# Optimization experiments

Measured on AMD Instinct MI355X. Metric: run time of the kernel, lower is better.

The kernel has to match this reference:

```python
import jax, jax.numpy as jnp
import numpy as np

N_NODES, N_EDGES, D_IN, D_HID, D_OUT = 100000, 3200000, 128, 64, 10


def _gcn_norm(src, dst, n):
    # symmetric normalization deg^{-1/2}[src] * deg^{-1/2}[dst]; edge weights = 1
    ones = jnp.ones(src.shape[0], jnp.float32)
    deg = jax.ops.segment_sum(ones, dst, num_segments=n)
    dinv = jnp.where(deg > 0, jax.lax.rsqrt(jnp.maximum(deg, 1.0)), 0.0)
    return dinv[src] * dinv[dst]


def _gcn_conv(x, W, b, src, dst, norm, n):
    h = x @ W                                   # [N, out]
    msg = norm[:, None] * jnp.take(h, src, axis=0)  # [E+N, out]
    return jax.ops.segment_sum(msg, dst, num_segments=n) + b


def setup_inputs() -> dict:
    key = jax.random.key(0)
    ks = jax.random.split(key, 8)
    x = jax.random.normal(ks[0], (N_NODES, D_IN), jnp.float32)
    edge_index = jax.random.randint(ks[1], (2, N_EDGES), 0, N_NODES, jnp.int32)
    def glorot(k, fan_in, fan_out):
        s = (6.0 / (fan_in + fan_out)) ** 0.5
        return jax.random.uniform(k, (fan_in, fan_out), jnp.float32, -s, s)
    return {
        "x": x,
        "edge_index": edge_index,
        "W1": glorot(ks[2], D_IN, D_HID), "b1": jnp.zeros((D_HID,), jnp.float32),
        "W2": glorot(ks[3], D_HID, D_HID), "b2": jnp.zeros((D_HID,), jnp.float32),
        "W3": glorot(ks[4], D_HID, D_OUT), "b3": jnp.zeros((D_OUT,), jnp.float32),
    }


def reference(x, edge_index, W1, b1, W2, b2, W3, b3):
    n = x.shape[0]
    loops = jnp.arange(n, dtype=edge_index.dtype)
    src = jnp.concatenate([edge_index[0], loops])  # add self-loops (PyG default)
    dst = jnp.concatenate([edge_index[1], loops])
    norm = _gcn_norm(src, dst, n)                  # identical for all 3 layers
    h = jax.nn.relu(_gcn_conv(x, W1, b1, src, dst, norm, n))
    h = jax.nn.relu(_gcn_conv(h, W2, b2, src, dst, norm, n))
    return _gcn_conv(h, W3, b3, src, dst, norm, n)
```

## Files before the change

kernel.cpp:

```cpp
#include <hip/hip_runtime.h>


constexpr int BK_SHIFT = 6;
constexpr int BK_NODES = 64;
constexpr int BK_CAP   = 2432;
constexpr int MAXNB    = 1568;

typedef __attribute__((ext_vector_type(8))) short short8_t;
typedef __attribute__((ext_vector_type(4))) float f32x4_t;

__device__ __forceinline__ unsigned short f2bf(float f) {
    unsigned u = __builtin_bit_cast(unsigned, f);
    u += 0x7FFF + ((u >> 16) & 1);
    return (unsigned short)(u >> 16);
}
__device__ __forceinline__ unsigned pack2(float lo, float hi) {
    return (unsigned)f2bf(lo) | ((unsigned)f2bf(hi) << 16);
}
__device__ __forceinline__ float bf_lo(unsigned d) {
    return __builtin_bit_cast(float, d << 16);
}
__device__ __forceinline__ float bf_hi(unsigned d) {
    return __builtin_bit_cast(float, d & 0xFFFF0000u);
}

__global__ void k_cursor_init(int* __restrict__ cursor, int nb) {
    int i = blockIdx.x * blockDim.x + threadIdx.x;
    if (i < nb) cursor[i] = i * BK_CAP;
}

__global__ void k_partition(const int* __restrict__ src, const int* __restrict__ dst,
                            int E, int nb, int* __restrict__ cursor,
                            unsigned* __restrict__ inter) {
    __shared__ int lcount[MAXNB];
    __shared__ int gbase[MAXNB];
    int t = threadIdx.x;
    int base = blockIdx.x * 16384;
    for (int i = t; i < MAXNB; i += 512) lcount[i] = 0;
    __syncthreads();
    int sv[32], dvv[32];
#pragma unroll
    for (int j = 0; j < 32; j++) {
        int idx = base + j * 512 + t;
        if (idx < E) {
            sv[j] = src[idx]; dvv[j] = dst[idx];
            atomicAdd(&lcount[dvv[j] >> BK_SHIFT], 1);
        } else dvv[j] = -1;
    }
    __syncthreads();
    for (int i = t; i < nb; i += 512) {
        int c = lcount[i]; int g = 0;
        if (c) g = atomicAdd(&cursor[i], c);
        gbase[i] = g; lcount[i] = 0;
    }
    __syncthreads();
#pragma unroll
    for (int j = 0; j < 32; j++) {
        if (dvv[j] >= 0) {
            int b = dvv[j] >> BK_SHIFT;
            int r = atomicAdd(&lcount[b], 1);
            int pos = gbase[b] + r;
            if (pos < (b + 1) * BK_CAP)
                inter[pos] = (unsigned)sv[j] | ((unsigned)(dvv[j] & (BK_NODES - 1)) << 20);
        }
    }
}

__global__ void k_dinvb(const unsigned* __restrict__ inter, const int* __restrict__ cursor,
                        float* __restrict__ dinv, int N) {
    __shared__ int hist[BK_NODES];
    int t = threadIdx.x, b = blockIdx.x;
    if (t < BK_NODES) hist[t] = 0;
    __syncthreads();
    int start = b * BK_CAP;
    int cnt = min(cursor[b] - start, BK_CAP);
    for (int i = t; i < cnt; i += 256) atomicAdd(&hist[inter[start + i] >> 20], 1);
    __syncthreads();
    if (t < BK_NODES) {
        int d = b * BK_NODES + t;
        if (d < N) dinv[d] = rsqrtf((float)(hist[t] + 1));
    }
}

template <int K, bool IN_F32>
__global__ __launch_bounds__(256) void k_gemmMF(const void* __restrict__ Xv,
                           const float* __restrict__ W,
                           const float* __restrict__ dinv,
                           unsigned short* __restrict__ Y, int n) {
    constexpr int KP = K + 8;
    __shared__ unsigned short Al[64 * KP];
    __shared__ unsigned short Bl[64 * KP];
    int t = threadIdx.x;
    int nb = blockIdx.x * 64;
    if (IN_F32) {
        const float* X = (const float*)Xv;
        for (int i = t * 4; i < 64 * K; i += 1024) {
            int r = i / K, c = i % K;
            int node = nb + r;
            float4 v = {0.f, 0.f, 0.f, 0.f};
            if (node < n) v = *reinterpret_cast<const float4*>(X + (size_t)node * K + c);
            uint2 pk = {pack2(v.x, v.y), pack2(v.z, v.w)};
            *reinterpret_cast<uint2*>(&Al[r * KP + c]) = pk;
        }
    } else {
        const unsigned short* X = (const unsigned short*)Xv;
        for (int i = t * 4; i < 64 * K; i += 1024) {
            int r = i / K, c = i % K;
            int node = nb + r;
            uint2 pk = {0u, 0u};
            if (node < n) pk = *reinterpret_cast<const uint2*>(X + (size_t)node * K + c);
            *reinterpret_cast<uint2*>(&Al[r * KP + c]) = pk;
        }
    }
    {
        int c = t & 63, kb = t >> 6;
        for (int k = kb; k < K; k += 4)
            Bl[c * KP + k] = f2bf(W[k * 64 + c]);
    }
    __syncthreads();
    int w = t >> 6, lane = t & 63;
    int ml = lane & 15, kg = lane >> 4;
    f32x4_t acc[4] = {{0,0,0,0},{0,0,0,0},{0,0,0,0},{0,0,0,0}};
    for (int ks = 0; ks < K / 32; ks++) {
        int ko = ks * 32 + kg * 8;
        short8_t a = *reinterpret_cast<const short8_t*>(&Al[(16 * w + ml) * KP + ko]);
#pragma unroll
        for (int c = 0; c < 4; c++) {
            short8_t b = *reinterpret_cast<const short8_t*>(&Bl[(16 * c + ml) * KP + ko]);
            acc[c] = __builtin_amdgcn_mfma_f32_16x16x32_bf16(a, b, acc[c], 0, 0, 0);
        }
    }
#pragma unroll
    for (int r = 0; r < 4; r++) {
        int grow = nb + 16 * w + kg * 4 + r;
        if (grow < n) {
            float dv = dinv[grow];
#pragma unroll
            for (int c = 0; c < 4; c++)
                Y[(size_t)grow * 64 + 16 * c + ml] = f2bf(dv * acc[c][r]);
        }
    }
}

__global__ void k_gemm10(const float* __restrict__ X, const float* __restrict__ W,
                         const float* __restrict__ dinv, float* __restrict__ Y, int n) {
    __shared__ float ws[64 * 10];
    __shared__ float xs[16 * 64];
    int t = threadIdx.x;
    for (int i = t; i < 640; i += 256) ws[i] = W[i];
    int nb = blockIdx.x * 16;
    for (int i = t; i < 16 * 64; i += 256) {
        int r = i >> 6, c = i & 63;
        int node = nb + r;
        xs[i] = (node < n) ? X[(size_t)node * 64 + c] : 0.f;
    }
    __syncthreads();
    int ns = t >> 4, c = t & 15;
    if (c < 10) {
        float acc = 0.f;
        for (int k = 0; k < 64; k++) acc += xs[ns * 64 + k] * ws[k * 10 + c];
        int node = nb + ns;
        if (node < n) Y[(size_t)node * 10 + c] = dinv[node] * acc;
    }
}

template <int OBF>
__global__ __launch_bounds__(512) void k_agg64(const unsigned short* __restrict__ H,
                        const unsigned* __restrict__ inter, const int* __restrict__ cursor,
                        const float* __restrict__ bias, void* __restrict__ outv,
                        int N, int relu) {
    __shared__ unsigned raw[BK_CAP];
    __shared__ unsigned srt[BK_CAP];
    __shared__ int hist[BK_NODES];
    __shared__ int offs[BK_NODES + 1];
    __shared__ int cur[BK_NODES];
    int t = threadIdx.x, b = blockIdx.x;
    if (t < BK_NODES) hist[t] = 0;
    __syncthreads();
    int start = b * BK_CAP;
    int cnt = min(cursor[b] - start, BK_CAP);
    for (int i = t; i < cnt; i += 512) {
        unsigned r = inter[start + i];
        raw[i] = r;
        atomicAdd(&hist[r >> 20], 1);
    }
    __syncthreads();
    if (t < BK_NODES) {
        int v = hist[t];
        int inc = v;
#pragma unroll
        for (int d = 1; d < 64; d <<= 1) {
            int o = __shfl_up(inc, d);
            if (t >= d) inc += o;
        }
        offs[t + 1] = inc;
        if (t == 0) offs[0] = 0;
        cur[t] = inc - v;
    }
    __syncthreads();
    for (int i = t; i < cnt; i += 512) {
        unsigned r = raw[i];
        int pos = atomicAdd(&cur[r >> 20], 1);
        srt[pos] = r & 0xFFFFFu;
    }
    __syncthreads();
    int wv = t >> 6, lane = t & 63;
    int esub = lane >> 3, cg = lane & 7;
    const unsigned short* Hc = H + (cg << 3);
    for (int nd = wv; nd < BK_NODES; nd += 8) {
        int d = b * BK_NODES + nd;
        if (d >= N) break;
        int o0 = offs[nd], o1 = offs[nd + 1];
        float a0 = 0.f, a1 = 0.f, a2 = 0.f, a3 = 0.f;
        float a4 = 0.f, a5 = 0.f, a6 = 0.f, a7 = 0.f;
        int e = o0 + esub;
        for (; e + 24 < o1; e += 32) {
            int s0 = srt[e], s1 = srt[e + 8], s2 = srt[e + 16], s3 = srt[e + 24];
            const uint4 v0 = *reinterpret_cast<const uint4*>(Hc + ((size_t)s0 << 6));
            const uint4 v1 = *reinterpret_cast<const uint4*>(Hc + ((size_t)s1 << 6));
            const uint4 v2 = *reinterpret_cast<const uint4*>(Hc + ((size_t)s2 << 6));
            const uint4 v3 = *reinterpret_cast<const uint4*>(Hc + ((size_t)s3 << 6));
            a0 += bf_lo(v0.x); a1 += bf_hi(v0.x); a2 += bf_lo(v0.y); a3 += bf_hi(v0.y);
            a4 += bf_lo(v0.z); a5 += bf_hi(v0.z); a6 += bf_lo(v0.w); a7 += bf_hi(v0.w);
            a0 += bf_lo(v1.x); a1 += bf_hi(v1.x); a2 += bf_lo(v1.y); a3 += bf_hi(v1.y);
            a4 += bf_lo(v1.z); a5 += bf_hi(v1.z); a6 += bf_lo(v1.w); a7 += bf_hi(v1.w);
            a0 += bf_lo(v2.x); a1 += bf_hi(v2.x); a2 += bf_lo(v2.y); a3 += bf_hi(v2.y);
            a4 += bf_lo(v2.z); a5 += bf_hi(v2.z); a6 += bf_lo(v2.w); a7 += bf_hi(v2.w);
            a0 += bf_lo(v3.x); a1 += bf_hi(v3.x); a2 += bf_lo(v3.y); a3 += bf_hi(v3.y);
            a4 += bf_lo(v3.z); a5 += bf_hi(v3.z); a6 += bf_lo(v3.w); a7 += bf_hi(v3.w);
        }
        for (; e < o1; e += 8) {
            int s0 = srt[e];
            const uint4 v0 = *reinterpret_cast<const uint4*>(Hc + ((size_t)s0 << 6));
            a0 += bf_lo(v0.x); a1 += bf_hi(v0.x); a2 += bf_lo(v0.y); a3 += bf_hi(v0.y);
            a4 += bf_lo(v0.z); a5 += bf_hi(v0.z); a6 += bf_lo(v0.w); a7 += bf_hi(v0.w);
        }
#pragma unroll
        for (int m = 8; m <= 32; m <<= 1) {
            a0 += __shfl_xor(a0, m); a1 += __shfl_xor(a1, m);
            a2 += __shfl_xor(a2, m); a3 += __shfl_xor(a3, m);
            a4 += __shfl_xor(a4, m); a5 += __shfl_xor(a5, m);
            a6 += __shfl_xor(a6, m); a7 += __shfl_xor(a7, m);
        }
        if (esub == 0) {
            float dv = rsqrtf((float)(hist[nd] + 1));
            const uint4 sv = *reinterpret_cast<const uint4*>(Hc + ((size_t)d << 6));
            float s[8] = {bf_lo(sv.x), bf_hi(sv.x), bf_lo(sv.y), bf_hi(sv.y),
                          bf_lo(sv.z), bf_hi(sv.z), bf_lo(sv.w), bf_hi(sv.w)};
            float acc[8] = {a0, a1, a2, a3, a4, a5, a6, a7};
            const float* bp = bias + cg * 8;
            float o[8];
#pragma unroll
            for (int j = 0; j < 8; j++) {
                float val = dv * (acc[j] + s[j]) + bp[j];
                if (relu) val = fmaxf(val, 0.f);
                o[j] = val;
            }
            if (OBF) {
                unsigned short* op = (unsigned short*)outv + (size_t)d * 64 + cg * 8;
                uint4 pk = {pack2(o[0], o[1]), pack2(o[2], o[3]),
                            pack2(o[4], o[5]), pack2(o[6], o[7])};
                *reinterpret_cast<uint4*>(op) = pk;
            } else {
                float* op = (float*)outv + (size_t)d * 64 + cg * 8;
                float4 r0 = {o[0], o[1], o[2], o[3]}, r1 = {o[4], o[5], o[6], o[7]};
                *reinterpret_cast<float4*>(op)     = r0;
                *reinterpret_cast<float4*>(op + 4) = r1;
            }
        }
    }
}

__global__ __launch_bounds__(512) void k_agg10(const float* __restrict__ H,
                        const unsigned* __restrict__ inter, const int* __restrict__ cursor,
                        const float* __restrict__ b3, float* __restrict__ out, int N) {
    __shared__ unsigned raw[BK_CAP];
    __shared__ unsigned srt[BK_CAP];
    __shared__ int hist[BK_NODES];
    __shared__ int offs[BK_NODES + 1];
    __shared__ int cur[BK_NODES];
    int t = threadIdx.x, b = blockIdx.x;
    if (t < BK_NODES) hist[t] = 0;
    __syncthreads();
    int start = b * BK_CAP;
    int cnt = min(cursor[b] - start, BK_CAP);
    for (int i = t; i < cnt; i += 512) {
        unsigned r = inter[start + i];
        raw[i] = r;
        atomicAdd(&hist[r >> 20], 1);
    }
    __syncthreads();
    if (t < BK_NODES) {
        int v = hist[t];
        int inc = v;
#pragma unroll
        for (int d = 1; d < 64; d <<= 1) {
            int o = __shfl_up(inc, d);
            if (t >= d) inc += o;
        }
        offs[t + 1] = inc;
        if (t == 0) offs[0] = 0;
        cur[t] = inc - v;
    }
    __syncthreads();
    for (int i = t; i < cnt; i += 512) {
        unsigned r = raw[i];
        int pos = atomicAdd(&cur[r >> 20], 1);
        srt[pos] = r & 0xFFFFFu;
    }
    __syncthreads();
    int wv = t >> 6, lane = t & 63;
    int esub = lane >> 4, c = lane & 15;
    for (int nd = wv; nd < BK_NODES; nd += 8) {
        int d = b * BK_NODES + nd;
        if (d >= N) break;
        int o0 = offs[nd], o1 = offs[nd + 1];
        float acc = 0.f;
        if (c < 10) {
            int e = o0 + esub;
            for (; e + 12 < o1; e += 16) {
                int s0 = srt[e], s1 = srt[e + 4], s2 = srt[e + 8], s3 = srt[e + 12];
                float h0 = H[(size_t)s0 * 10 + c], h1 = H[(size_t)s1 * 10 + c];
                float h2 = H[(size_t)s2 * 10 + c], h3 = H[(size_t)s3 * 10 + c];
                acc += (h0 + h1) + (h2 + h3);
            }
            for (; e < o1; e += 4) acc += H[(size_t)srt[e] * 10 + c];
        }
        acc += __shfl_xor(acc, 16);
        acc += __shfl_xor(acc, 32);
        if (esub == 0 && c < 10) {
            float dv = rsqrtf((float)(hist[nd] + 1));
            out[(size_t)d * 10 + c] = dv * (acc + H[(size_t)d * 10 + c]) + b3[c];
        }
    }
}

extern "C" void kernel_launch(void* const* d_in, const int* in_sizes, int n_in,
                              void* d_out, int out_size, void* d_ws, size_t ws_size,
                              hipStream_t stream) {
    const float* x  = (const float*)d_in[0];
    const int*   ei = (const int*)d_in[1];
    const float* W1 = (const float*)d_in[2];
    const float* b1 = (const float*)d_in[3];
    const float* W2 = (const float*)d_in[4];
    const float* b2 = (const float*)d_in[5];
    const float* W3 = (const float*)d_in[6];
    const float* b3 = (const float*)d_in[7];

    int N = in_sizes[0] / 128;
    int E = in_sizes[1] / 2;
    const int* esrc = ei;
    const int* edst = ei + E;
    int nb = (N + BK_NODES - 1) >> BK_SHIFT;

    char* p = (char*)d_ws;
    auto carve = [&](size_t bytes) -> void* {
        void* r = p;
        p += (bytes + 255) & ~(size_t)255;
        return r;
    };
    int*      cursor = (int*)carve((size_t)MAXNB * 4);
    unsigned* inter  = (unsigned*)carve((size_t)nb * BK_CAP * 4);
    float*    dinv   = (float*)carve((size_t)N * 4);
    unsigned short* Hs = (unsigned short*)carve((size_t)N * 64 * 2);
    unsigned short* Gb = (unsigned short*)carve((size_t)N * 64 * 2);
    float*    Gf     = (float*)carve((size_t)N * 64 * 4);
    float*    Hs10   = (float*)carve((size_t)N * 10 * 4);
    (void)ws_size; (void)n_in; (void)out_size;

    k_cursor_init<<<(nb + 255) / 256, 256, 0, stream>>>(cursor, nb);
    k_partition<<<(E + 16383) / 16384, 512, 0, stream>>>(esrc, edst, E, nb, cursor, inter);
    k_dinvb<<<nb, 256, 0, stream>>>(inter, cursor, dinv, N);

    k_gemmMF<128, true><<<(N + 63) / 64, 256, 0, stream>>>(x, W1, dinv, Hs, N);
    k_agg64<1><<<nb, 512, 0, stream>>>(Hs, inter, cursor, b1, Gb, N, 1);
    k_gemmMF<64, false><<<(N + 63) / 64, 256, 0, stream>>>(Gb, W2, dinv, Hs, N);
    k_agg64<0><<<nb, 512, 0, stream>>>(Hs, inter, cursor, b2, Gf, N, 1);
    k_gemm10<<<(N + 15) / 16, 256, 0, stream>>>(Gf, W3, dinv, Hs10, N);
    k_agg10<<<nb, 512, 0, stream>>>(Hs10, inter, cursor, b3, (float*)d_out, N);
}
```

Before: 254.1 us.

## Store layer-3 features in bf16, memset cursors, reduce agg unrolling

Stores the 10-wide layer-3 transformed features as bf16 instead of fp32, halving the bytes gathered per edge in the final aggregation. The cursor-init kernel is replaced by a memset, with bucket offsets now computed relative to each bucket base. The gather loops in the 64-wide and 10-wide aggregation kernels are unrolled less, which lowers register pressure but leaves fewer loads in flight. The bf16 features add rounding error to the final layer.

Result: faster. 246.0 us (-3.2%).

```diff
diff --git a/kernel.cpp b/kernel.cpp
--- a/kernel.cpp
+++ b/kernel.cpp
@@ -23,10 +23,8 @@
 __device__ __forceinline__ float bf_hi(unsigned d) {
     return __builtin_bit_cast(float, d & 0xFFFF0000u);
 }
-
-__global__ void k_cursor_init(int* __restrict__ cursor, int nb) {
-    int i = blockIdx.x * blockDim.x + threadIdx.x;
-    if (i < nb) cursor[i] = i * BK_CAP;
+__device__ __forceinline__ float bf1(unsigned short u) {
+    return __builtin_bit_cast(float, (unsigned)u << 16);
 }
 
 __global__ void k_partition(const int* __restrict__ src, const int* __restrict__ dst,
@@ -58,10 +56,10 @@
     for (int j = 0; j < 32; j++) {
         if (dvv[j] >= 0) {
             int b = dvv[j] >> BK_SHIFT;
-            int r = atomicAdd(&lcount[b], 1);
-            int pos = gbase[b] + r;
-            if (pos < (b + 1) * BK_CAP)
-                inter[pos] = (unsigned)sv[j] | ((unsigned)(dvv[j] & (BK_NODES - 1)) << 20);
+            int r = gbase[b] + atomicAdd(&lcount[b], 1);
+            if (r < BK_CAP)
+                inter[(size_t)b * BK_CAP + r] =
+                    (unsigned)sv[j] | ((unsigned)(dvv[j] & (BK_NODES - 1)) << 20);
         }
     }
 }
@@ -72,9 +70,9 @@
     int t = threadIdx.x, b = blockIdx.x;
     if (t < BK_NODES) hist[t] = 0;
     __syncthreads();
-    int start = b * BK_CAP;
-    int cnt = min(cursor[b] - start, BK_CAP);
-    for (int i = t; i < cnt; i += 256) atomicAdd(&hist[inter[start + i] >> 20], 1);
+    int cnt = min(cursor[b], BK_CAP);
+    const unsigned* ip = inter + (size_t)b * BK_CAP;
+    for (int i = t; i < cnt; i += 256) atomicAdd(&hist[ip[i] >> 20], 1);
     __syncthreads();
     if (t < BK_NODES) {
         int d = b * BK_NODES + t;
@@ -143,7 +141,7 @@
 }
 
 __global__ void k_gemm10(const float* __restrict__ X, const float* __restrict__ W,
-                         const float* __restrict__ dinv, float* __restrict__ Y, int n) {
+                         const float* __restrict__ dinv, unsigned short* __restrict__ Y, int n) {
     __shared__ float ws[64 * 10];
     __shared__ float xs[16 * 64];
     int t = threadIdx.x;
@@ -160,7 +158,7 @@
         float acc = 0.f;
         for (int k = 0; k < 64; k++) acc += xs[ns * 64 + k] * ws[k * 10 + c];
         int node = nb + ns;
-        if (node < n) Y[(size_t)node * 10 + c] = dinv[node] * acc;
+        if (node < n) Y[(size_t)node * 10 + c] = f2bf(dinv[node] * acc);
     }
 }
 
@@ -177,10 +175,10 @@
     int t = threadIdx.x, b = blockIdx.x;
     if (t < BK_NODES) hist[t] = 0;
     __syncthreads();
-    int start = b * BK_CAP;
-    int cnt = min(cursor[b] - start, BK_CAP);
+    int cnt = min(cursor[b], BK_CAP);
+    const unsigned* ip = inter + (size_t)b * BK_CAP;
     for (int i = t; i < cnt; i += 512) {
-        unsigned r = inter[start + i];
+        unsigned r = ip[i];
         raw[i] = r;
         atomicAdd(&hist[r >> 20], 1);
     }
@@ -214,20 +212,14 @@
         float a0 = 0.f, a1 = 0.f, a2 = 0.f, a3 = 0.f;
         float a4 = 0.f, a5 = 0.f, a6 = 0.f, a7 = 0.f;
         int e = o0 + esub;
-        for (; e + 24 < o1; e += 32) {
-            int s0 = srt[e], s1 = srt[e + 8], s2 = srt[e + 16], s3 = srt[e + 24];
+        for (; e + 8 < o1; e += 16) {
+            int s0 = srt[e], s1 = srt[e + 8];
             const uint4 v0 = *reinterpret_cast<const uint4*>(Hc + ((size_t)s0 << 6));
             const uint4 v1 = *reinterpret_cast<const uint4*>(Hc + ((size_t)s1 << 6));
-            const uint4 v2 = *reinterpret_cast<const uint4*>(Hc + ((size_t)s2 << 6));
-            const uint4 v3 = *reinterpret_cast<const uint4*>(Hc + ((size_t)s3 << 6));
             a0 += bf_lo(v0.x); a1 += bf_hi(v0.x); a2 += bf_lo(v0.y); a3 += bf_hi(v0.y);
             a4 += bf_lo(v0.z); a5 += bf_hi(v0.z); a6 += bf_lo(v0.w); a7 += bf_hi(v0.w);
             a0 += bf_lo(v1.x); a1 += bf_hi(v1.x); a2 += bf_lo(v1.y); a3 += bf_hi(v1.y);
             a4 += bf_lo(v1.z); a5 += bf_hi(v1.z); a6 += bf_lo(v1.w); a7 += bf_hi(v1.w);
-            a0 += bf_lo(v2.x); a1 += bf_hi(v2.x); a2 += bf_lo(v2.y); a3 += bf_hi(v2.y);
-            a4 += bf_lo(v2.z); a5 += bf_hi(v2.z); a6 += bf_lo(v2.w); a7 += bf_hi(v2.w);
-            a0 += bf_lo(v3.x); a1 += bf_hi(v3.x); a2 += bf_lo(v3.y); a3 += bf_hi(v3.y);
-            a4 += bf_lo(v3.z); a5 += bf_hi(v3.z); a6 += bf_lo(v3.w); a7 += bf_hi(v3.w);
         }
         for (; e < o1; e += 8) {
             int s0 = srt[e];
@@ -271,7 +263,7 @@
     }
 }
 
-__global__ __launch_bounds__(512) void k_agg10(const float* __restrict__ H,
+__global__ __launch_bounds__(512) void k_agg10(const unsigned short* __restrict__ H,
                         const unsigned* __restrict__ inter, const int* __restrict__ cursor,
                         const float* __restrict__ b3, float* __restrict__ out, int N) {
     __shared__ unsigned raw[BK_CAP];
@@ -282,10 +274,10 @@
     int t = threadIdx.x, b = blockIdx.x;
     if (t < BK_NODES) hist[t] = 0;
     __syncthreads();
-    int start = b * BK_CAP;
-    int cnt = min(cursor[b] - start, BK_CAP);
+    int cnt = min(cursor[b], BK_CAP);
+    const unsigned* ip = inter + (size_t)b * BK_CAP;
     for (int i = t; i < cnt; i += 512) {
-        unsigned r = inter[start + i];
+        unsigned r = ip[i];
         raw[i] = r;
         atomicAdd(&hist[r >> 20], 1);
     }
@@ -318,19 +310,17 @@
         float acc = 0.f;
         if (c < 10) {
             int e = o0 + esub;
-            for (; e + 12 < o1; e += 16) {
-                int s0 = srt[e], s1 = srt[e + 4], s2 = srt[e + 8], s3 = srt[e + 12];
-                float h0 = H[(size_t)s0 * 10 + c], h1 = H[(size_t)s1 * 10 + c];
-                float h2 = H[(size_t)s2 * 10 + c], h3 = H[(size_t)s3 * 10 + c];
-                acc += (h0 + h1) + (h2 + h3);
+            for (; e + 4 < o1; e += 8) {
+                int s0 = srt[e], s1 = srt[e + 4];
+                acc += bf1(H[(size_t)s0 * 10 + c]) + bf1(H[(size_t)s1 * 10 + c]);
             }
-            for (; e < o1; e += 4) acc += H[(size_t)srt[e] * 10 + c];
+            if (e < o1) acc += bf1(H[(size_t)srt[e] * 10 + c]);
         }
         acc += __shfl_xor(acc, 16);
         acc += __shfl_xor(acc, 32);
         if (esub == 0 && c < 10) {
             float dv = rsqrtf((float)(hist[nd] + 1));
-            out[(size_t)d * 10 + c] = dv * (acc + H[(size_t)d * 10 + c]) + b3[c];
+            out[(size_t)d * 10 + c] = dv * (acc + bf1(H[(size_t)d * 10 + c])) + b3[c];
         }
     }
 }
@@ -365,10 +355,10 @@
     unsigned short* Hs = (unsigned short*)carve((size_t)N * 64 * 2);
     unsigned short* Gb = (unsigned short*)carve((size_t)N * 64 * 2);
     float*    Gf     = (float*)carve((size_t)N * 64 * 4);
-    float*    Hs10   = (float*)carve((size_t)N * 10 * 4);
+    unsigned short* Hs10 = (unsigned short*)carve((size_t)N * 10 * 2);
     (void)ws_size; (void)n_in; (void)out_size;
 
-    k_cursor_init<<<(nb + 255) / 256, 256, 0, stream>>>(cursor, nb);
+    hipMemsetAsync(cursor, 0, (size_t)nb * 4, stream);
     k_partition<<<(E + 16383) / 16384, 512, 0, stream>>>(esrc, edst, E, nb, cursor, inter);
     k_dinvb<<<nb, 256, 0, stream>>>(inter, cursor, dinv, N);
 
```
